# Performance work log

Measured on AMD Instinct MI355X. Metric: run time of the kernel, lower is better.

The kernel has to match this reference:

```python
import jax, jax.numpy as jnp
import numpy as np

B, P, H = 32768, 128, 64

def setup_inputs() -> dict:
    key = jax.random.key(0)
    ks = jax.random.split(key, 6)
    planet_xy = jax.random.normal(ks[0], (B, P, 2), dtype=jnp.float32)
    planet_m = jax.random.uniform(ks[1], (P,), dtype=jnp.float32)
    ast_xy = jax.random.normal(ks[2], (B, 2), dtype=jnp.float32)
    W1 = jax.random.normal(ks[3], (4, H), dtype=jnp.float32) * 0.5
    b1 = jnp.zeros((H,), dtype=jnp.float32)
    W2 = jax.random.normal(ks[4], (H, H), dtype=jnp.float32) * 0.125
    b2 = jnp.zeros((H,), dtype=jnp.float32)
    return {"planet_xy": planet_xy, "planet_m": planet_m, "ast_xy": ast_xy,
            "W1": W1, "b1": b1, "W2": W2, "b2": b2}

def reference(planet_xy, planet_m, ast_xy, W1, b1, W2, b2):
    # d: (B, P, 2) broadcast difference planet - asteroid
    d = planet_xy - ast_xy[:, None, :]
    dist2 = jnp.sum(d * d, axis=-1) + 1e-6            # (B, P)
    invdist = 1.0 / jnp.sqrt(dist2)                   # (B, P)
    m = jnp.broadcast_to(planet_m[None, :], dist2.shape)  # (B, P)
    feats = jnp.concatenate([d, invdist[..., None], m[..., None]], axis=-1)  # (B, P, 4)
    h = jax.nn.relu(jnp.einsum('bpf,fh->bph', feats, W1) + b1)  # (B, P, H)
    msg = jax.nn.relu(jnp.einsum('bph,hk->bpk', h, W2) + b2)    # (B, P, H)
    return msg.sum(axis=1)                             # (B, H)
```

## Files before the change

### kernel.cpp

```cpp
#include <hip/hip_runtime.h>
#include <hip/hip_fp16.h>

#define NP    128
#define NH    64
#define RST   18
#define ITERS 4
#define WPB   4

typedef __attribute__((ext_vector_type(8))) _Float16 f16x8;
typedef __attribute__((ext_vector_type(4))) _Float16 f16x4;
typedef __attribute__((ext_vector_type(2))) __fp16  hf16x2;
typedef __attribute__((ext_vector_type(4))) float f32x4;

union FragK16 { f16x4 v; unsigned int u[2]; };
union FragK32 { f16x8 v; unsigned int u[4]; };

__device__ __forceinline__ unsigned int pack_pkrtz(float a, float b) {
    hf16x2 t = __builtin_amdgcn_cvt_pkrtz(a, b);
    return __builtin_bit_cast(unsigned int, t);
}

__device__ __forceinline__ unsigned int relu2_pk(unsigned int u) {
    hf16x2 h = __builtin_bit_cast(hf16x2, u);
    h = __builtin_elementwise_max(h, (hf16x2)(__fp16)0.f);
    return __builtin_bit_cast(unsigned int, h);
}

__global__ void __launch_bounds__(256, 2) gnn_wave(
    const float* __restrict__ planet_xy,
    const float* __restrict__ planet_m,
    const float* __restrict__ ast_xy,
    const float* __restrict__ W1,
    const float* __restrict__ b1,
    const float* __restrict__ W2,
    const float* __restrict__ b2,
    float* __restrict__ out)
{
    __shared__ float rsum[WPB][64 * RST];

    const int tid  = threadIdx.x;
    const int wv   = tid >> 6;
    const int lane = tid & 63;
    const int q    = lane >> 4;
    const int lm   = lane & 15;
    const bool q0  = (q == 0);
    const bool q1  = (q == 1);

    FragK16 w1f[4];
    #pragma unroll
    for (int mt = 0; mt < 4; mt++) {
        const int m = 16 * mt + lm;
        float wa = W1[0 * NH + m], wb = W1[1 * NH + m];
        float wc = W1[2 * NH + m], wd = W1[3 * NH + m];
        float be = b1[m];
        w1f[mt].u[0] = q0 ? pack_pkrtz(wa, wb) : (q1 ? pack_pkrtz(be, 0.f) : 0u);
        w1f[mt].u[1] = q0 ? pack_pkrtz(wc, wd) : 0u;
    }

    FragK32 w2a[4][2];
    #pragma unroll
    for (int np = 0; np < 4; np++)
        #pragma unroll
        for (int kk = 0; kk < 2; kk++) {
            const int n = 16 * np + lm;
            const int k0 = 32 * kk + 4 * q;
            const int k1 = 32 * kk + 16 + 4 * q;
            w2a[np][kk].u[0] = pack_pkrtz(W2[(k0 + 0) * NH + n], W2[(k0 + 1) * NH + n]);
            w2a[np][kk].u[1] = pack_pkrtz(W2[(k0 + 2) * NH + n], W2[(k0 + 3) * NH + n]);
            w2a[np][kk].u[2] = pack_pkrtz(W2[(k1 + 0) * NH + n], W2[(k1 + 1) * NH + n]);
            w2a[np][kk].u[3] = pack_pkrtz(W2[(k1 + 2) * NH + n], W2[(k1 + 3) * NH + n]);
        }

    f32x4 b2f[4];
    #pragma unroll
    for (int np = 0; np < 4; np++)
        b2f[np] = *(const f32x4*)&b2[16 * np + 4 * q];

    float pmv[8];
    #pragma unroll
    for (int i = 0; i < 8; i++)
        pmv[i] = planet_m[16 * i + lm];

    const unsigned int bf0_const = q1 ? pack_pkrtz(1.f, 0.f) : 0u;
    const f32x4 zf = (f32x4){0.f, 0.f, 0.f, 0.f};

    int b = (blockIdx.x * WPB + wv) * ITERS;

    for (int it = 0; it < ITERS; ++it, ++b) {
        const float2 axy = *(const float2*)&ast_xy[2 * b];
        float2 pxy[8];
        #pragma unroll
        for (int i = 0; i < 8; i++)
            pxy[i] = *(const float2*)&planet_xy[((size_t)b * NP + 16 * i + lm) * 2];

        f32x4 sums[4];
        #pragma unroll
        for (int np = 0; np < 4; np++)
            sums[np] = zf;

        #pragma unroll
        for (int mi = 0; mi < 8; ++mi) {
            float dx = pxy[mi].x - axy.x, dy = pxy[mi].y - axy.y;
            float inv = __builtin_amdgcn_rsqf(fmaf(dx, dx, fmaf(dy, dy, 1e-6f)));
            FragK16 bf;
            bf.u[0] = q0 ? pack_pkrtz(dx, dy)        : bf0_const;
            bf.u[1] = q0 ? pack_pkrtz(inv, pmv[mi])  : 0u;

            FragK16 hb[4];
            #pragma unroll
            for (int mt = 0; mt < 4; mt++) {
                f32x4 c = __builtin_amdgcn_mfma_f32_16x16x16f16(w1f[mt].v, bf.v, zf, 0, 0, 0);
                hb[mt].u[0] = relu2_pk(pack_pkrtz(c[0], c[1]));
                hb[mt].u[1] = relu2_pk(pack_pkrtz(c[2], c[3]));
            }

            FragK32 hB[2];
            #pragma unroll
            for (int kk = 0; kk < 2; kk++) {
                hB[kk].u[0] = hb[2 * kk + 0].u[0];
                hB[kk].u[1] = hb[2 * kk + 0].u[1];
                hB[kk].u[2] = hb[2 * kk + 1].u[0];
                hB[kk].u[3] = hb[2 * kk + 1].u[1];
            }

            #pragma unroll
            for (int np = 0; np < 4; np++) {
                f32x4 acc = __builtin_amdgcn_mfma_f32_16x16x32_f16(w2a[np][0].v, hB[0].v, b2f[np], 0, 0, 0);
                acc = __builtin_amdgcn_mfma_f32_16x16x32_f16(w2a[np][1].v, hB[1].v, acc, 0, 0, 0);
                sums[np] += __builtin_elementwise_max(acc, zf);
            }
        }

        #pragma unroll
        for (int np = 0; np < 4; np++)
            #pragma unroll
            for (int r = 0; r < 4; r++)
                rsum[wv][(16 * np + 4 * q + r) * RST + lm] = sums[np][r];

        float tot = 0.f;
        #pragma unroll
        for (int i = 0; i < 8; i++) {
            float2 v = *(const float2*)&rsum[wv][lane * RST + 2 * i];
            tot += v.x + v.y;
        }
        out[(size_t)b * NH + lane] = tot;
    }
}

extern "C" void kernel_launch(void* const* d_in, const int* in_sizes, int n_in,
                              void* d_out, int out_size, void* d_ws, size_t ws_size,
                              hipStream_t stream) {
    const float* planet_xy = (const float*)d_in[0];
    const float* planet_m  = (const float*)d_in[1];
    const float* ast_xy    = (const float*)d_in[2];
    const float* W1        = (const float*)d_in[3];
    const float* b1        = (const float*)d_in[4];
    const float* W2        = (const float*)d_in[5];
    const float* b2        = (const float*)d_in[6];
    float* outp            = (float*)d_out;

    const int B = in_sizes[2] / 2;
    const int batches_per_block = WPB * ITERS;
    const int grid = (B + batches_per_block - 1) / batches_per_block;

    gnn_wave<<<grid, 256, 0, stream>>>(planet_xy, planet_m, ast_xy, W1, b1, W2, b2, outp);
}
```

Measured before the change: 129.7 us.

## Double-buffer planet loads across batches and interleave two MFMA chains

```diff
diff --git a/kernel.cpp b/kernel.cpp
--- a/kernel.cpp
+++ b/kernel.cpp
@@ -4,7 +4,7 @@
 #define NP    128
 #define NH    64
 #define RST   18
-#define ITERS 4
+#define ITERS 8
 #define WPB   4
 
 typedef __attribute__((ext_vector_type(8))) _Float16 f16x8;
@@ -34,7 +34,8 @@
     const float* __restrict__ b1,
     const float* __restrict__ W2,
     const float* __restrict__ b2,
-    float* __restrict__ out)
+    float* __restrict__ out,
+    int B)
 {
     __shared__ float rsum[WPB][64 * RST];
 
@@ -84,67 +85,80 @@
     const unsigned int bf0_const = q1 ? pack_pkrtz(1.f, 0.f) : 0u;
     const f32x4 zf = (f32x4){0.f, 0.f, 0.f, 0.f};
 
-    int b = (blockIdx.x * WPB + wv) * ITERS;
+    const int b0 = (blockIdx.x * WPB + wv) * ITERS;
+    const int bMax = B - 1;
 
-    for (int it = 0; it < ITERS; ++it, ++b) {
-        const float2 axy = *(const float2*)&ast_xy[2 * b];
-        float2 pxy[8];
+    float2 pxyA[8], pxyB[8];
+    float2 axyA, axyB;
+    {
+        const int bl = (b0 <= bMax) ? b0 : bMax;
         #pragma unroll
         for (int i = 0; i < 8; i++)
-            pxy[i] = *(const float2*)&planet_xy[((size_t)b * NP + 16 * i + lm) * 2];
+            pxyA[i] = *(const float2*)&planet_xy[((size_t)bl * NP + 16 * i + lm) * 2];
+        axyA = *(const float2*)&ast_xy[2 * bl];
+    }
 
-        f32x4 sums[4];
-        #pragma unroll
-        for (int np = 0; np < 4; np++)
-            sums[np] = zf;
+#define GNN_BODY(PCUR, PNXT, AXY, AXYN, BB, BN)                                     \
+    {                                                                               \
+        const int bn_ = ((BN) <= bMax) ? (BN) : bMax;                               \
+        _Pragma("unroll")                                                           \
+        for (int i = 0; i < 8; i++)                                                 \
+            PNXT[i] = *(const float2*)&planet_xy[((size_t)bn_ * NP + 16 * i + lm) * 2]; \
+        AXYN = *(const float2*)&ast_xy[2 * bn_];                                    \
+        f32x4 sums[4];                                                              \
+        _Pragma("unroll")                                                           \
+        for (int np = 0; np < 4; np++) sums[np] = zf;                               \
+        _Pragma("unroll")                                                           \
+        for (int mi = 0; mi < 8; mi += 2) {                                         \
+            float dxa = PCUR[mi].x - AXY.x,     dya = PCUR[mi].y - AXY.y;           \
+            float dxb = PCUR[mi + 1].x - AXY.x, dyb = PCUR[mi + 1].y - AXY.y;       \
+            float inva = __builtin_amdgcn_rsqf(fmaf(dxa, dxa, fmaf(dya, dya, 1e-6f))); \
+            float invb = __builtin_amdgcn_rsqf(fmaf(dxb, dxb, fmaf(dyb, dyb, 1e-6f))); \
+            FragK16 bfa, bfb;                                                       \
+            bfa.u[0] = q0 ? pack_pkrtz(dxa, dya)          : bf0_const;              \
+            bfa.u[1] = q0 ? pack_pkrtz(inva, pmv[mi])     : 0u;                     \
+            bfb.u[0] = q0 ? pack_pkrtz(dxb, dyb)          : bf0_const;              \
+            bfb.u[1] = q0 ? pack_pkrtz(invb, pmv[mi + 1]) : 0u;                     \
+            FragK32 hBa[2], hBb[2];                                                 \
+            _Pragma("unroll")                                                       \
+            for (int mt = 0; mt < 4; mt++) {                                        \
+                f32x4 ca = __builtin_amdgcn_mfma_f32_16x16x16f16(w1f[mt].v, bfa.v, zf, 0, 0, 0); \
+                f32x4 cb = __builtin_amdgcn_mfma_f32_16x16x16f16(w1f[mt].v, bfb.v, zf, 0, 0, 0); \
+                hBa[mt >> 1].u[(mt & 1) * 2 + 0] = relu2_pk(pack_pkrtz(ca[0], ca[1])); \
+                hBa[mt >> 1].u[(mt & 1) * 2 + 1] = relu2_pk(pack_pkrtz(ca[2], ca[3])); \
+                hBb[mt >> 1].u[(mt & 1) * 2 + 0] = relu2_pk(pack_pkrtz(cb[0], cb[1])); \
+                hBb[mt >> 1].u[(mt & 1) * 2 + 1] = relu2_pk(pack_pkrtz(cb[2], cb[3])); \
+            }                                                                       \
+            _Pragma("unroll")                                                       \
+            for (int np = 0; np < 4; np++) {                                        \
+                f32x4 acca = __builtin_amdgcn_mfma_f32_16x16x32_f16(w2a[np][0].v, hBa[0].v, b2f[np], 0, 0, 0); \
+                f32x4 accb = __builtin_amdgcn_mfma_f32_16x16x32_f16(w2a[np][0].v, hBb[0].v, b2f[np], 0, 0, 0); \
+                acca = __builtin_amdgcn_mfma_f32_16x16x32_f16(w2a[np][1].v, hBa[1].v, acca, 0, 0, 0); \
+                accb = __builtin_amdgcn_mfma_f32_16x16x32_f16(w2a[np][1].v, hBb[1].v, accb, 0, 0, 0); \
+                sums[np] += __builtin_elementwise_max(acca, zf);                    \
+                sums[np] += __builtin_elementwise_max(accb, zf);                    \
+            }                                                                       \
+        }                                                                           \
+        _Pragma("unroll")                                                           \
+        for (int np = 0; np < 4; np++)                                              \
+            _Pragma("unroll")                                                       \
+            for (int r = 0; r < 4; r++)                                             \
+                rsum[wv][(16 * np + 4 * q + r) * RST + lm] = sums[np][r];           \
+        float tot = 0.f;                                                            \
+        _Pragma("unroll")                                                           \
+        for (int i = 0; i < 8; i++) {                                               \
+            float2 v2 = *(const float2*)&rsum[wv][lane * RST + 2 * i];              \
+            tot += v2.x + v2.y;                                                     \
+        }                                                                           \
+        if ((BB) <= bMax) out[(size_t)(BB) * NH + lane] = tot;                      \
+    }
 
-        #pragma unroll
-        for (int mi = 0; mi < 8; ++mi) {
-            float dx = pxy[mi].x - axy.x, dy = pxy[mi].y - axy.y;
-            float inv = __builtin_amdgcn_rsqf(fmaf(dx, dx, fmaf(dy, dy, 1e-6f)));
-            FragK16 bf;
-            bf.u[0] = q0 ? pack_pkrtz(dx, dy)        : bf0_const;
-            bf.u[1] = q0 ? pack_pkrtz(inv, pmv[mi])  : 0u;
-
-            FragK16 hb[4];
-            #pragma unroll
-            for (int mt = 0; mt < 4; mt++) {
-                f32x4 c = __builtin_amdgcn_mfma_f32_16x16x16f16(w1f[mt].v, bf.v, zf, 0, 0, 0);
-                hb[mt].u[0] = relu2_pk(pack_pkrtz(c[0], c[1]));
-                hb[mt].u[1] = relu2_pk(pack_pkrtz(c[2], c[3]));
-            }
-
-            FragK32 hB[2];
-            #pragma unroll
-            for (int kk = 0; kk < 2; kk++) {
-                hB[kk].u[0] = hb[2 * kk + 0].u[0];
-                hB[kk].u[1] = hb[2 * kk + 0].u[1];
-                hB[kk].u[2] = hb[2 * kk + 1].u[0];
-                hB[kk].u[3] = hb[2 * kk + 1].u[1];
-            }
-
-            #pragma unroll
-            for (int np = 0; np < 4; np++) {
-                f32x4 acc = __builtin_amdgcn_mfma_f32_16x16x32_f16(w2a[np][0].v, hB[0].v, b2f[np], 0, 0, 0);
-                acc = __builtin_amdgcn_mfma_f32_16x16x32_f16(w2a[np][1].v, hB[1].v, acc, 0, 0, 0);
-                sums[np] += __builtin_elementwise_max(acc, zf);
-            }
-        }
-
-        #pragma unroll
-        for (int np = 0; np < 4; np++)
-            #pragma unroll
-            for (int r = 0; r < 4; r++)
-                rsum[wv][(16 * np + 4 * q + r) * RST + lm] = sums[np][r];
-
-        float tot = 0.f;
-        #pragma unroll
-        for (int i = 0; i < 8; i++) {
-            float2 v = *(const float2*)&rsum[wv][lane * RST + 2 * i];
-            tot += v.x + v.y;
-        }
-        out[(size_t)b * NH + lane] = tot;
+    for (int it2 = 0; it2 < ITERS; it2 += 2) {
+        const int b = b0 + it2;
+        GNN_BODY(pxyA, pxyB, axyA, axyB, b, b + 1);
+        GNN_BODY(pxyB, pxyA, axyB, axyA, b + 1, b + 2);
     }
+#undef GNN_BODY
 }
 
 extern "C" void kernel_launch(void* const* d_in, const int* in_sizes, int n_in,
@@ -163,5 +177,5 @@
     const int batches_per_block = WPB * ITERS;
     const int grid = (B + batches_per_block - 1) / batches_per_block;
 
-    gnn_wave<<<grid, 256, 0, stream>>>(planet_xy, planet_m, ast_xy, W1, b1, W2, b2, outp);
+    gnn_wave<<<grid, 256, 0, stream>>>(planet_xy, planet_m, ast_xy, W1, b1, W2, b2, outp, B);
 }
```

Result: slower. 132.7 us (+2.4%).
